# Optimization experiments

Hardware: AMD Instinct MI355X
Metric: run time of the kernel (lower is better)

The kernel has to match this reference:

```python
import jax, jax.numpy as jnp
import numpy as np

S, N, E = 12, 16384, 262144        # timesteps, nodes, edges per timestep
DIN = DOUT = H = 128               # gcn in/out dim == lstm hidden (required by module)
B = 64                             # batch_size; N % B == 0


def setup_inputs() -> dict:
    key = jax.random.key(0)
    ks = jax.random.split(key, 10)
    return {
        "adj_indices": jax.random.randint(ks[0], (S, 2, E), 0, N, dtype=jnp.int32),
        "adj_values": jax.random.uniform(ks[1], (S, E), dtype=jnp.float32),
        "xs": jax.random.normal(ks[2], (S, N, DIN), dtype=jnp.float32),
        "gcn_weight": jax.random.normal(ks[3], (DIN, DOUT), dtype=jnp.float32) * 0.05,
        "gcn_bias": jnp.zeros((DOUT,), jnp.float32),
        "w_ih": jax.random.normal(ks[4], (4 * H, DOUT), dtype=jnp.float32) * 0.05,
        "w_hh": jax.random.normal(ks[5], (4 * H, H), dtype=jnp.float32) * 0.05,
        "b_ih": jnp.zeros((4 * H,), jnp.float32),
        "b_hh": jnp.zeros((4 * H,), jnp.float32),
        "h0": jax.random.normal(ks[6], (B, H), dtype=jnp.float32),
        "c0": jax.random.normal(ks[7], (B, H), dtype=jnp.float32),
    }


def reference(adj_indices, adj_values, xs, gcn_weight, gcn_bias,
              w_ih, w_hh, b_ih, b_hh, h0, c0):
    # --- GCN per timestep: relu(sparse_A @ (X @ W) + b) ---
    def gcn(idx, vals, x):
        support = x @ gcn_weight                      # [N, DOUT]
        msg = vals[:, None] * support[idx[1]]         # gather cols -> [E, DOUT]
        out = jax.ops.segment_sum(msg, idx[0], num_segments=N)  # scatter rows
        return jax.nn.relu(out + gcn_bias)

    cur = jax.vmap(gcn)(adj_indices, adj_values, xs)  # [S, N, DOUT]
    seq = cur.reshape(-1, B, DOUT)                    # [T=S*N/B, B, H]

    # --- single-layer LSTM (torch gate order: i, f, g, o) ---
    def step(carry, x_t):
        h, c = carry
        gates = x_t @ w_ih.T + b_ih + h @ w_hh.T + b_hh   # [B, 4H]
        i, f, g, o = jnp.split(gates, 4, axis=-1)
        c = jax.nn.sigmoid(f) * c + jax.nn.sigmoid(i) * jnp.tanh(g)
        h = jax.nn.sigmoid(o) * jnp.tanh(c)
        return (h, c), h

    _, hs = jax.lax.scan(step, (h0, c0), seq)         # [T, B, H]
    return hs
```

## Files before the change

### kernel.cpp

```cpp
#include <hip/hip_runtime.h>
#include <cstdint>
#include <cstddef>

#define SS 12
#define NN 16384
#define EE 262144
#define TT 3072

typedef _Float16 h2_t __attribute__((ext_vector_type(2)));
typedef short bf16x8 __attribute__((ext_vector_type(8)));
typedef float floatx4 __attribute__((ext_vector_type(4)));
typedef unsigned short ushortx8 __attribute__((ext_vector_type(8)));

__device__ __forceinline__ float fast_sig(float x) {
    float e = __builtin_amdgcn_exp2f(-1.442695041f * x);
    return __builtin_amdgcn_rcpf(1.f + e);
}
__device__ __forceinline__ float fast_tanh(float x) {
    float e = __builtin_amdgcn_exp2f(2.885390082f * x);
    return 1.f - 2.f * __builtin_amdgcn_rcpf(e + 1.f);
}
__device__ __forceinline__ unsigned short f2bf(float f) {
    unsigned int x = __float_as_uint(f);
    unsigned int r = (x + 0x7FFFu + ((x >> 16) & 1u)) >> 16;
    return (unsigned short)r;
}
__device__ __forceinline__ float bf2f(unsigned short u) {
    return __uint_as_float(((unsigned int)u) << 16);
}
__device__ __forceinline__ float dpp_xor1(float x) {
    int i = __builtin_amdgcn_mov_dpp(__float_as_int(x), 0xB1, 0xF, 0xF, true);
    return __int_as_float(i);
}
__device__ __forceinline__ float dpp_xor2(float x) {
    int i = __builtin_amdgcn_mov_dpp(__float_as_int(x), 0x4E, 0xF, 0xF, true);
    return __int_as_float(i);
}

__global__ void k_zero(int* __restrict__ p) {
    p[blockIdx.x * 256 + threadIdx.x] = 0;
}

__global__ void k_count(const int* __restrict__ adj, int* __restrict__ counts) {
    int i = blockIdx.x * 256 + threadIdx.x;
    int t = i / EE, e = i - t * EE;
    int dst = adj[(size_t)t * 2 * EE + e];
    atomicAdd(&counts[t * NN + dst], 1);
}

__global__ void k_scan(const int* __restrict__ counts, int* __restrict__ offs,
                       int* __restrict__ cursor) {
    __shared__ int sums[1024];
    int t = blockIdx.x, tid = threadIdx.x;
    const int per = NN / 1024;
    int base = t * NN + tid * per;
    int local[16];
    int s = 0;
#pragma unroll
    for (int i = 0; i < per; i++) { local[i] = counts[base + i]; s += local[i]; }
    sums[tid] = s;
    __syncthreads();
    for (int off = 1; off < 1024; off <<= 1) {
        int v = (tid >= off) ? sums[tid - off] : 0;
        __syncthreads();
        sums[tid] += v;
        __syncthreads();
    }
    int run = sums[tid] - s;
#pragma unroll
    for (int i = 0; i < per; i++) { offs[base + i] = run; cursor[base + i] = run; run += local[i]; }
}

__global__ void k_scatter(const int* __restrict__ adj, const float* __restrict__ vals,
                          int* __restrict__ cursor, int2* __restrict__ edges) {
    int i = blockIdx.x * 256 + threadIdx.x;
    int t = i / EE, e = i - t * EE;
    int dst = adj[(size_t)t * 2 * EE + e];
    int src = adj[(size_t)t * 2 * EE + EE + e];
    float v = vals[(size_t)t * EE + e];
    int p = atomicAdd(&cursor[t * NN + dst], 1);
    edges[(size_t)t * EE + p] = make_int2(src, __float_as_int(v));
}

__global__ __launch_bounds__(256) void k_support(const float* __restrict__ xs,
                                                 const float* __restrict__ W,
                                                 unsigned short* __restrict__ sup) {
    __shared__ float Ash[64][128];
    __shared__ float Wsh[128][128];
    int tid = threadIdx.x;
    size_t rowbase = (size_t)blockIdx.x * 64;
    const float4* xa = (const float4*)(xs + rowbase * 128);
    float4* As = (float4*)&Ash[0][0];
#pragma unroll
    for (int q = 0; q < 8; q++) As[tid + q * 256] = xa[tid + q * 256];
    const float4* wg = (const float4*)W;
    float4* Ws = (float4*)&Wsh[0][0];
#pragma unroll
    for (int q = 0; q < 16; q++) Ws[tid + q * 256] = wg[tid + q * 256];
    __syncthreads();
    int jg = tid & 31, rg = tid >> 5;
    float acc[8][4];
#pragma unroll
    for (int i = 0; i < 8; i++)
#pragma unroll
        for (int j = 0; j < 4; j++) acc[i][j] = 0.f;
    for (int k4 = 0; k4 < 128; k4 += 4) {
        float4 a[8];
#pragma unroll
        for (int i = 0; i < 8; i++) a[i] = *(const float4*)&Ash[rg * 8 + i][k4];
#pragma unroll
        for (int kk = 0; kk < 4; kk++) {
            float4 wv = *(const float4*)&Wsh[k4 + kk][jg * 4];
#pragma unroll
            for (int i = 0; i < 8; i++) {
                float av = (kk == 0) ? a[i].x : (kk == 1) ? a[i].y : (kk == 2) ? a[i].z : a[i].w;
                acc[i][0] += av * wv.x; acc[i][1] += av * wv.y;
                acc[i][2] += av * wv.z; acc[i][3] += av * wv.w;
            }
        }
    }
#pragma unroll
    for (int i = 0; i < 8; i++) {
        ushort4 o;
        o.x = f2bf(acc[i][0]); o.y = f2bf(acc[i][1]);
        o.z = f2bf(acc[i][2]); o.w = f2bf(acc[i][3]);
        *(ushort4*)&sup[(rowbase + rg * 8 + i) * 128 + jg * 4] = o;
    }
}

__global__ __launch_bounds__(256) void k_gather(const int2* __restrict__ edges,
                         const int* __restrict__ offs,
                         const int* __restrict__ ends,
                         const unsigned short* __restrict__ sup,
                         const float* __restrict__ bias,
                         unsigned short* __restrict__ cur) {
    int bn = blockIdx.x * 4 + (threadIdx.x >> 6);
    bn = __builtin_amdgcn_readfirstlane(bn);
    int t = bn >> 14;
    int l = threadIdx.x & 63;
    int beg = offs[bn];
    int end = ends[bn];
    const unsigned short* supt = sup + (size_t)t * NN * 128;
    const int2* eg = edges + (size_t)t * EE;
    float acc0 = 0.f, acc1 = 0.f;
    int p = beg;
    for (; p + 3 < end; p += 4) {
        int2 e0 = eg[p], e1 = eg[p + 1], e2 = eg[p + 2], e3 = eg[p + 3];
        unsigned int u0 = *(const unsigned int*)&supt[(size_t)e0.x * 128 + 2 * l];
        unsigned int u1 = *(const unsigned int*)&supt[(size_t)e1.x * 128 + 2 * l];
        unsigned int u2 = *(const unsigned int*)&supt[(size_t)e2.x * 128 + 2 * l];
        unsigned int u3 = *(const unsigned int*)&supt[(size_t)e3.x * 128 + 2 * l];
        float w0 = __int_as_float(e0.y), w1 = __int_as_float(e1.y);
        float w2 = __int_as_float(e2.y), w3 = __int_as_float(e3.y);
        acc0 += w0 * bf2f((unsigned short)u0); acc1 += w0 * bf2f((unsigned short)(u0 >> 16));
        acc0 += w1 * bf2f((unsigned short)u1); acc1 += w1 * bf2f((unsigned short)(u1 >> 16));
        acc0 += w2 * bf2f((unsigned short)u2); acc1 += w2 * bf2f((unsigned short)(u2 >> 16));
        acc0 += w3 * bf2f((unsigned short)u3); acc1 += w3 * bf2f((unsigned short)(u3 >> 16));
    }
    for (; p < end; p++) {
        int2 e0 = eg[p];
        unsigned int u0 = *(const unsigned int*)&supt[(size_t)e0.x * 128 + 2 * l];
        float w0 = __int_as_float(e0.y);
        acc0 += w0 * bf2f((unsigned short)u0);
        acc1 += w0 * bf2f((unsigned short)(u0 >> 16));
    }
    float r0 = acc0 + bias[2 * l];
    float r1 = acc1 + bias[2 * l + 1];
    ushort2 o;
    o.x = f2bf(r0 > 0.f ? r0 : 0.f);
    o.y = f2bf(r1 > 0.f ? r1 : 0.f);
    *(ushort2*)&cur[(size_t)bn * 128 + 2 * l] = o;
}

__global__ __launch_bounds__(256) void k_xgates(const unsigned short* __restrict__ cur,
                                                const float* __restrict__ wih,
                                                const float* __restrict__ bih,
                                                const float* __restrict__ bhh,
                                                unsigned short* __restrict__ gx) {
    __shared__ __align__(16) unsigned short At[64][136];
    __shared__ __align__(16) unsigned short Bt[64][136];
    int tid = threadIdx.x;
    size_t rowbase = (size_t)blockIdx.x * 64;
    int gbase = blockIdx.y * 64;
#pragma unroll
    for (int q = 0; q < 4; q++) {
        int idx = tid + q * 256;
        int r = idx >> 4;
        int cc = (idx & 15) * 8;
        *(ushortx8*)&At[r][cc] = *(const ushortx8*)&cur[(rowbase + r) * 128 + cc];
    }
#pragma unroll
    for (int q = 0; q < 8; q++) {
        int idx = tid + q * 256;
        int r = idx >> 5;
        int c4 = (idx & 31) * 4;
        float4 v = *(const float4*)&wih[(size_t)(gbase + r) * 128 + c4];
        ushort4 o;
        o.x = f2bf(v.x); o.y = f2bf(v.y); o.z = f2bf(v.z); o.w = f2bf(v.w);
        *(ushort4*)&Bt[r][c4] = o;
    }
    __syncthreads();
    int wave = tid >> 6, lane = tid & 63;
    int m0 = wave * 16;
    int rin = lane & 15;
    int koff = (lane >> 4) * 8;
    floatx4 acc[4];
#pragma unroll
    for (int n = 0; n < 4; n++) acc[n] = (floatx4){0.f, 0.f, 0.f, 0.f};
#pragma unroll
    for (int kc = 0; kc < 4; kc++) {
        bf16x8 a = *(const bf16x8*)&At[m0 + rin][kc * 32 + koff];
#pragma unroll
        for (int n = 0; n < 4; n++) {
            bf16x8 b = *(const bf16x8*)&Bt[n * 16 + rin][kc * 32 + koff];
            acc[n] = __builtin_amdgcn_mfma_f32_16x16x32_bf16(a, b, acc[n], 0, 0, 0);
        }
    }
    int rq = (lane >> 4) * 4;
#pragma unroll
    for (int n = 0; n < 4; n++) {
        int gcol = gbase + n * 16 + rin;
        float bs = bih[gcol] + bhh[gcol];
        int slot = ((gcol & 127) << 2) | (gcol >> 7);
#pragma unroll
        for (int i = 0; i < 4; i++) {
            size_t row = rowbase + m0 + rq + i;
            gx[row * 512 + slot] = f2bf(acc[n][i] + bs);
        }
    }
}

__global__ __launch_bounds__(256, 1) void k_lstm(const unsigned short* __restrict__ gx,
                                                 const float* __restrict__ whh,
                                                 const float* __restrict__ h0,
                                                 const float* __restrict__ c0,
                                                 float* __restrict__ out) {
    __shared__ __align__(16) _Float16 hsh[2][128];
    int b = blockIdx.x, tid = threadIdx.x;
    int Q = tid >> 2;
    int ll = tid & 3;
    int p = (tid >> 1) & 1;
    int j = 2 * Q + p;

    h2_t wreg[8][16];
#pragma unroll
    for (int g8 = 0; g8 < 8; g8++) {
        int row = (g8 & 3) * 128 + 2 * Q + (g8 >> 2);
        const float4* rp = (const float4*)(whh + (size_t)row * 128 + ll * 32);
#pragma unroll
        for (int q4 = 0; q4 < 8; q4++) {
            float4 v = rp[q4];
            h2_t a; a.x = (_Float16)v.x; a.y = (_Float16)v.y;
            h2_t bq; bq.x = (_Float16)v.z; bq.y = (_Float16)v.w;
            wreg[g8][2 * q4] = a; wreg[g8][2 * q4 + 1] = bq;
        }
    }
    float c = c0[(size_t)b * 128 + j];
    if (tid < 128) hsh[0][tid] = (_Float16)h0[(size_t)b * 128 + tid];
    __syncthreads();

    const unsigned short* gxb = gx + (size_t)b * 512 + 4 * j;
    uint2 rg0 = *(const uint2*)(gxb);
    uint2 rg1 = *(const uint2*)(gxb + 32768);
    uint2 rg2 = *(const uint2*)(gxb + 2 * (size_t)32768);

#define LSTM_STEP(T, RD, WR, QIDX)                                          \
    {                                                                       \
        const h2_t* hp_ = (const h2_t*)&hsh[RD][32 * ll];                   \
        h2_t hs_[16];                                                       \
        _Pragma("unroll")                                                   \
        for (int kk = 0; kk < 16; kk++) hs_[kk] = hp_[kk];                  \
        float part_[8];                                                     \
        _Pragma("unroll")                                                   \
        for (int g8 = 0; g8 < 8; g8++) part_[g8] = 0.f;                     \
        _Pragma("unroll")                                                   \
        for (int kk = 0; kk < 16; kk++) {                                   \
            _Pragma("unroll")                                               \
            for (int g8 = 0; g8 < 8; g8++)                                  \
                part_[g8] = __builtin_amdgcn_fdot2(wreg[g8][kk], hs_[kk],   \
                                                   part_[g8], false);       \
        }                                                                   \
        _Pragma("unroll")                                                   \
        for (int g8 = 0; g8 < 8; g8++) part_[g8] += dpp_xor1(part_[g8]);    \
        _Pragma("unroll")                                                   \
        for (int g8 = 0; g8 < 8; g8++) part_[g8] += dpp_xor2(part_[g8]);    \
        float si_ = p ? part_[4] : part_[0];                                \
        float sf_ = p ? part_[5] : part_[1];                                \
        float sg_ = p ? part_[6] : part_[2];                                \
        float so_ = p ? part_[7] : part_[3];                                \
        uint2 gv_ = rg0;                                                    \
        float ri_ = si_ + bf2f((unsigned short)(gv_.x & 0xffffu));          \
        float rf_ = sf_ + bf2f((unsigned short)(gv_.x >> 16));              \
        float rgg_ = sg_ + bf2f((unsigned short)(gv_.y & 0xffffu));         \
        float ro_ = so_ + bf2f((unsigned short)(gv_.y >> 16));              \
        float ai_ = fast_sig(ri_);                                          \
        float af_ = fast_sig(rf_);                                          \
        float ag_ = fast_tanh(rgg_);                                        \
        float ao_ = fast_sig(ro_);                                          \
        c = af_ * c + ai_ * ag_;                                            \
        float hn_ = ao_ * fast_tanh(c);                                     \
        hh8[QIDX] = hn_;                                                    \
        if ((tid & 1) == 0) hsh[WR][j] = (_Float16)hn_;                     \
        rg0 = rg1; rg1 = rg2;                                               \
        {                                                                   \
            int tp_ = ((T) + 3 < TT) ? (T) + 3 : TT - 1;                    \
            rg2 = *(const uint2*)(gxb + (size_t)tp_ * 32768);               \
        }                                                                   \
        __syncthreads();                                                    \
    }

    for (int t8 = 0; t8 < TT; t8 += 8) {
        float hh8[8];
        LSTM_STEP(t8 + 0, 0, 1, 0);
        LSTM_STEP(t8 + 1, 1, 0, 1);
        LSTM_STEP(t8 + 2, 0, 1, 2);
        LSTM_STEP(t8 + 3, 1, 0, 3);
        LSTM_STEP(t8 + 4, 0, 1, 4);
        LSTM_STEP(t8 + 5, 1, 0, 5);
        LSTM_STEP(t8 + 6, 0, 1, 6);
        LSTM_STEP(t8 + 7, 1, 0, 7);
        if ((tid & 1) == 0) {
#pragma unroll
            for (int q = 0; q < 8; q++)
                out[((size_t)(t8 + q) * 64 + b) * 128 + j] = hh8[q];
        }
    }
#undef LSTM_STEP
}

extern "C" void kernel_launch(void* const* d_in, const int* in_sizes, int n_in,
                              void* d_out, int out_size, void* d_ws, size_t ws_size,
                              hipStream_t stream) {
    const int* adj    = (const int*)d_in[0];
    const float* vals = (const float*)d_in[1];
    const float* xs   = (const float*)d_in[2];
    const float* gw   = (const float*)d_in[3];
    const float* gb   = (const float*)d_in[4];
    const float* wih  = (const float*)d_in[5];
    const float* whh  = (const float*)d_in[6];
    const float* bih  = (const float*)d_in[7];
    const float* bhh  = (const float*)d_in[8];
    const float* h0   = (const float*)d_in[9];
    const float* c0   = (const float*)d_in[10];
    float* out = (float*)d_out;

    char* ws = (char*)d_ws;
    unsigned short* cur = (unsigned short*)(ws);
    unsigned short* gx  = (unsigned short*)(ws + 50331648);
    unsigned short* sup = (unsigned short*)(ws + 50331648);
    int* counts         = (int*)(ws + 100663296);
    int* offs           = (int*)(ws + 101449728);
    int* cursor         = (int*)(ws + 102236160);
    int2* edges         = (int2*)(ws + 103022592);

    k_zero<<<(SS * NN) / 256, 256, 0, stream>>>(counts);
    k_count<<<(SS * EE) / 256, 256, 0, stream>>>(adj, counts);
    k_scan<<<SS, 1024, 0, stream>>>(counts, offs, cursor);
    k_scatter<<<(SS * EE) / 256, 256, 0, stream>>>(adj, vals, cursor, edges);
    k_support<<<(SS * NN) / 64, 256, 0, stream>>>(xs, gw, sup);
    k_gather<<<(SS * NN) / 4, 256, 0, stream>>>(edges, offs, cursor, sup, gb, cur);
    k_xgates<<<dim3((SS * NN) / 64, 8), 256, 0, stream>>>(cur, wih, bih, bhh, gx);
    k_lstm<<<64, 256, 0, stream>>>(gx, whh, h0, c0, out);
}
```

Before: 2.330 ms.

## Split LSTM recurrence across 512 threads with per-lane gate activation and DPP exchange

The recurrent LSTM kernel now launches 512 threads per batch row instead of 256. Each thread holds four W_hh row slices instead of eight, which halves the fdot2 work per thread on the serial critical path. Every lane applies one unified sigmoid/tanh activation to its own gate, and the four gate values are swapped between lanes with DPP moves, so each lane no longer computes four activations. In exchange the kernel needs more waves per block and so more per-step barrier synchronisation, and it issues narrower gate loads.

```diff
diff --git a/kernel.cpp b/kernel.cpp
--- a/kernel.cpp
+++ b/kernel.cpp
@@ -12,10 +12,6 @@
 typedef float floatx4 __attribute__((ext_vector_type(4)));
 typedef unsigned short ushortx8 __attribute__((ext_vector_type(8)));
 
-__device__ __forceinline__ float fast_sig(float x) {
-    float e = __builtin_amdgcn_exp2f(-1.442695041f * x);
-    return __builtin_amdgcn_rcpf(1.f + e);
-}
 __device__ __forceinline__ float fast_tanh(float x) {
     float e = __builtin_amdgcn_exp2f(2.885390082f * x);
     return 1.f - 2.f * __builtin_amdgcn_rcpf(e + 1.f);
@@ -34,6 +30,10 @@
 }
 __device__ __forceinline__ float dpp_xor2(float x) {
     int i = __builtin_amdgcn_mov_dpp(__float_as_int(x), 0x4E, 0xF, 0xF, true);
+    return __int_as_float(i);
+}
+__device__ __forceinline__ float dpp_xor3(float x) {
+    int i = __builtin_amdgcn_mov_dpp(__float_as_int(x), 0x1B, 0xF, 0xF, true);
     return __int_as_float(i);
 }
 
@@ -230,81 +230,77 @@
     }
 }
 
-__global__ __launch_bounds__(256, 1) void k_lstm(const unsigned short* __restrict__ gx,
+__global__ __launch_bounds__(512, 2) void k_lstm(const unsigned short* __restrict__ gx,
                                                  const float* __restrict__ whh,
                                                  const float* __restrict__ h0,
                                                  const float* __restrict__ c0,
                                                  float* __restrict__ out) {
     __shared__ __align__(16) _Float16 hsh[2][128];
     int b = blockIdx.x, tid = threadIdx.x;
-    int Q = tid >> 2;
-    int ll = tid & 3;
-    int p = (tid >> 1) & 1;
-    int j = 2 * Q + p;
-
-    h2_t wreg[8][16];
-#pragma unroll
-    for (int g8 = 0; g8 < 8; g8++) {
-        int row = (g8 & 3) * 128 + 2 * Q + (g8 >> 2);
-        const float4* rp = (const float4*)(whh + (size_t)row * 128 + ll * 32);
+    int j = tid >> 2;
+    int q = tid & 3;
+    float K1 = (q == 2) ? -2.885390082f : -1.442695041f;
+    float Aa = (q == 2) ? 2.f : 1.f;
+    float Bb = (q == 2) ? -1.f : 0.f;
+
+    h2_t w[4][16];
+#pragma unroll
+    for (int g = 0; g < 4; g++) {
+        const float4* rp = (const float4*)(whh + (size_t)(g * 128 + j) * 128 + q * 32);
 #pragma unroll
         for (int q4 = 0; q4 < 8; q4++) {
             float4 v = rp[q4];
             h2_t a; a.x = (_Float16)v.x; a.y = (_Float16)v.y;
             h2_t bq; bq.x = (_Float16)v.z; bq.y = (_Float16)v.w;
-            wreg[g8][2 * q4] = a; wreg[g8][2 * q4 + 1] = bq;
+            w[g][2 * q4] = a; w[g][2 * q4 + 1] = bq;
         }
     }
     float c = c0[(size_t)b * 128 + j];
     if (tid < 128) hsh[0][tid] = (_Float16)h0[(size_t)b * 128 + tid];
     __syncthreads();
 
-    const unsigned short* gxb = gx + (size_t)b * 512 + 4 * j;
-    uint2 rg0 = *(const uint2*)(gxb);
-    uint2 rg1 = *(const uint2*)(gxb + 32768);
-    uint2 rg2 = *(const uint2*)(gxb + 2 * (size_t)32768);
+    const unsigned short* gxb = gx + (size_t)b * 512 + tid;
+    unsigned short rg0 = gxb[0];
+    unsigned short rg1 = gxb[32768];
+    unsigned short rg2 = gxb[2 * (size_t)32768];
 
 #define LSTM_STEP(T, RD, WR, QIDX)                                          \
     {                                                                       \
-        const h2_t* hp_ = (const h2_t*)&hsh[RD][32 * ll];                   \
+        const h2_t* hp_ = (const h2_t*)&hsh[RD][32 * q];                    \
         h2_t hs_[16];                                                       \
         _Pragma("unroll")                                                   \
         for (int kk = 0; kk < 16; kk++) hs_[kk] = hp_[kk];                  \
-        float part_[8];                                                     \
-        _Pragma("unroll")                                                   \
-        for (int g8 = 0; g8 < 8; g8++) part_[g8] = 0.f;                     \
+        float part_[4];                                                     \
+        _Pragma("unroll")                                                   \
+        for (int g = 0; g < 4; g++) part_[g] = 0.f;                         \
         _Pragma("unroll")                                                   \
         for (int kk = 0; kk < 16; kk++) {                                   \
             _Pragma("unroll")                                               \
-            for (int g8 = 0; g8 < 8; g8++)                                  \
-                part_[g8] = __builtin_amdgcn_fdot2(wreg[g8][kk], hs_[kk],   \
-                                                   part_[g8], false);       \
+            for (int g = 0; g < 4; g++)                                     \
+                part_[g] = __builtin_amdgcn_fdot2(w[g][kk], hs_[kk],        \
+                                                  part_[g], false);         \
         }                                                                   \
         _Pragma("unroll")                                                   \
-        for (int g8 = 0; g8 < 8; g8++) part_[g8] += dpp_xor1(part_[g8]);    \
-        _Pragma("unroll")                                                   \
-        for (int g8 = 0; g8 < 8; g8++) part_[g8] += dpp_xor2(part_[g8]);    \
-        float si_ = p ? part_[4] : part_[0];                                \
-        float sf_ = p ? part_[5] : part_[1];                                \
-        float sg_ = p ? part_[6] : part_[2];                                \
-        float so_ = p ? part_[7] : part_[3];                                \
-        uint2 gv_ = rg0;                                                    \
-        float ri_ = si_ + bf2f((unsigned short)(gv_.x & 0xffffu));          \
-        float rf_ = sf_ + bf2f((unsigned short)(gv_.x >> 16));              \
-        float rgg_ = sg_ + bf2f((unsigned short)(gv_.y & 0xffffu));         \
-        float ro_ = so_ + bf2f((unsigned short)(gv_.y >> 16));              \
-        float ai_ = fast_sig(ri_);                                          \
-        float af_ = fast_sig(rf_);                                          \
-        float ag_ = fast_tanh(rgg_);                                        \
-        float ao_ = fast_sig(ro_);                                          \
-        c = af_ * c + ai_ * ag_;                                            \
-        float hn_ = ao_ * fast_tanh(c);                                     \
+        for (int g = 0; g < 4; g++) part_[g] += dpp_xor1(part_[g]);         \
+        _Pragma("unroll")                                                   \
+        for (int g = 0; g < 4; g++) part_[g] += dpp_xor2(part_[g]);         \
+        float s01_ = (q & 1) ? part_[1] : part_[0];                         \
+        float s23_ = (q & 1) ? part_[3] : part_[2];                         \
+        float sown_ = (q & 2) ? s23_ : s01_;                                \
+        float x_ = sown_ + bf2f(rg0);                                       \
+        float e_ = __builtin_amdgcn_exp2f(K1 * x_);                         \
+        float act_ = Aa * __builtin_amdgcn_rcpf(1.f + e_) + Bb;             \
+        float f_ = dpp_xor1(act_);                                          \
+        float tg_ = dpp_xor2(act_);                                         \
+        float o_ = dpp_xor3(act_);                                          \
+        c = f_ * c + act_ * tg_;                   \
+        float hn_ = o_ * fast_tanh(c);                                      \
         hh8[QIDX] = hn_;                                                    \
-        if ((tid & 1) == 0) hsh[WR][j] = (_Float16)hn_;                     \
+        if (q == 0) hsh[WR][j] = (_Float16)hn_;                             \
         rg0 = rg1; rg1 = rg2;                                               \
         {                                                                   \
             int tp_ = ((T) + 3 < TT) ? (T) + 3 : TT - 1;                    \
-            rg2 = *(const uint2*)(gxb + (size_t)tp_ * 32768);               \
+            rg2 = gxb[(size_t)tp_ * 32768];                                 \
         }                                                                   \
         __syncthreads();                                                    \
     }
@@ -319,10 +315,10 @@
         LSTM_STEP(t8 + 5, 1, 0, 5);
         LSTM_STEP(t8 + 6, 0, 1, 6);
         LSTM_STEP(t8 + 7, 1, 0, 7);
-        if ((tid & 1) == 0) {
-#pragma unroll
-            for (int q = 0; q < 8; q++)
-                out[((size_t)(t8 + q) * 64 + b) * 128 + j] = hh8[q];
+        if (q == 0) {
+#pragma unroll
+            for (int qq = 0; qq < 8; qq++)
+                out[((size_t)(t8 + qq) * 64 + b) * 128 + j] = hh8[qq];
         }
     }
 #undef LSTM_STEP
@@ -360,5 +356,5 @@
     k_support<<<(SS * NN) / 64, 256, 0, stream>>>(xs, gw, sup);
     k_gather<<<(SS * NN) / 4, 256, 0, stream>>>(edges, offs, cursor, sup, gb, cur);
     k_xgates<<<dim3((SS * NN) / 64, 8), 256, 0, stream>>>(cur, wih, bih, bhh, gx);
-    k_lstm<<<64, 256, 0, stream>>>(gx, whh, h0, c0, out);
-}
+    k_lstm<<<64, 512, 0, stream>>>(gx, whh, h0, c0, out);
+}
```

Measured after the change: 2.379 ms. +2.1%, slower.

## Compute LSTM recurrent matvec with MFMA using 512-thread blocks

Applied to the files above, without the earlier changes.

Replaces the per-thread fdot2 recurrent dot products and DPP cross-lane reductions in the LSTM kernel with MFMA 16x16x32 f16 instructions. The hidden state is broadcast as the A operand and only one output column of the result is used. Blocks grow to 512 threads (8 waves, 16 hidden units each), and each lane holds W_hh fragments as B operands. This targets the serial per-step latency of the recurrence, at the cost of wasted MFMA rows, and the larger block may make the per-step barrier more expensive.

```diff
diff --git a/kernel.cpp b/kernel.cpp
--- a/kernel.cpp
+++ b/kernel.cpp
@@ -8,6 +8,7 @@
 #define TT 3072
 
 typedef _Float16 h2_t __attribute__((ext_vector_type(2)));
+typedef _Float16 f16x8 __attribute__((ext_vector_type(8)));
 typedef short bf16x8 __attribute__((ext_vector_type(8)));
 typedef float floatx4 __attribute__((ext_vector_type(4)));
 typedef unsigned short ushortx8 __attribute__((ext_vector_type(8)));
@@ -27,14 +28,6 @@
 }
 __device__ __forceinline__ float bf2f(unsigned short u) {
     return __uint_as_float(((unsigned int)u) << 16);
-}
-__device__ __forceinline__ float dpp_xor1(float x) {
-    int i = __builtin_amdgcn_mov_dpp(__float_as_int(x), 0xB1, 0xF, 0xF, true);
-    return __int_as_float(i);
-}
-__device__ __forceinline__ float dpp_xor2(float x) {
-    int i = __builtin_amdgcn_mov_dpp(__float_as_int(x), 0x4E, 0xF, 0xF, true);
-    return __int_as_float(i);
 }
 
 __global__ void k_zero(int* __restrict__ p) {
@@ -230,29 +223,34 @@
     }
 }
 
-__global__ __launch_bounds__(256, 1) void k_lstm(const unsigned short* __restrict__ gx,
+__global__ __launch_bounds__(512, 2) void k_lstm(const unsigned short* __restrict__ gx,
                                                  const float* __restrict__ whh,
                                                  const float* __restrict__ h0,
                                                  const float* __restrict__ c0,
                                                  float* __restrict__ out) {
     __shared__ __align__(16) _Float16 hsh[2][128];
     int b = blockIdx.x, tid = threadIdx.x;
-    int Q = tid >> 2;
-    int ll = tid & 3;
-    int p = (tid >> 1) & 1;
-    int j = 2 * Q + p;
-
-    h2_t wreg[8][16];
-#pragma unroll
-    for (int g8 = 0; g8 < 8; g8++) {
-        int row = (g8 & 3) * 128 + 2 * Q + (g8 >> 2);
-        const float4* rp = (const float4*)(whh + (size_t)row * 128 + ll * 32);
-#pragma unroll
-        for (int q4 = 0; q4 < 8; q4++) {
-            float4 v = rp[q4];
-            h2_t a; a.x = (_Float16)v.x; a.y = (_Float16)v.y;
-            h2_t bq; bq.x = (_Float16)v.z; bq.y = (_Float16)v.w;
-            wreg[g8][2 * q4] = a; wreg[g8][2 * q4 + 1] = bq;
+    int w = tid >> 6;
+    int l = tid & 63;
+    int col = l & 15;
+    int kg = l >> 4;
+    int j = w * 16 + col;
+
+    f16x8 bw[4][4];
+#pragma unroll
+    for (int n = 0; n < 4; n++) {
+        const float* rp = whh + (size_t)(n * 128 + j) * 128;
+#pragma unroll
+        for (int kt = 0; kt < 4; kt++) {
+            int k0 = kt * 32 + kg * 8;
+            float4 v0 = *(const float4*)(rp + k0);
+            float4 v1 = *(const float4*)(rp + k0 + 4);
+            f16x8 f;
+            f[0] = (_Float16)v0.x; f[1] = (_Float16)v0.y;
+            f[2] = (_Float16)v0.z; f[3] = (_Float16)v0.w;
+            f[4] = (_Float16)v1.x; f[5] = (_Float16)v1.y;
+            f[6] = (_Float16)v1.z; f[7] = (_Float16)v1.w;
+            bw[n][kt] = f;
         }
     }
     float c = c0[(size_t)b * 128 + j];
@@ -266,41 +264,42 @@
 
 #define LSTM_STEP(T, RD, WR, QIDX)                                          \
     {                                                                       \
-        const h2_t* hp_ = (const h2_t*)&hsh[RD][32 * ll];                   \
-        h2_t hs_[16];                                                       \
-        _Pragma("unroll")                                                   \
-        for (int kk = 0; kk < 16; kk++) hs_[kk] = hp_[kk];                  \
-        float part_[8];                                                     \
-        _Pragma("unroll")                                                   \
-        for (int g8 = 0; g8 < 8; g8++) part_[g8] = 0.f;                     \
-        _Pragma("unroll")                                                   \
-        for (int kk = 0; kk < 16; kk++) {                                   \
-            _Pragma("unroll")                                               \
-            for (int g8 = 0; g8 < 8; g8++)                                  \
-                part_[g8] = __builtin_amdgcn_fdot2(wreg[g8][kk], hs_[kk],   \
-                                                   part_[g8], false);       \
-        }                                                                   \
-        _Pragma("unroll")                                                   \
-        for (int g8 = 0; g8 < 8; g8++) part_[g8] += dpp_xor1(part_[g8]);    \
-        _Pragma("unroll")                                                   \
-        for (int g8 = 0; g8 < 8; g8++) part_[g8] += dpp_xor2(part_[g8]);    \
-        float si_ = p ? part_[4] : part_[0];                                \
-        float sf_ = p ? part_[5] : part_[1];                                \
-        float sg_ = p ? part_[6] : part_[2];                                \
-        float so_ = p ? part_[7] : part_[3];                                \
-        uint2 gv_ = rg0;                                                    \
-        float ri_ = si_ + bf2f((unsigned short)(gv_.x & 0xffffu));          \
-        float rf_ = sf_ + bf2f((unsigned short)(gv_.x >> 16));              \
-        float rgg_ = sg_ + bf2f((unsigned short)(gv_.y & 0xffffu));         \
-        float ro_ = so_ + bf2f((unsigned short)(gv_.y >> 16));              \
+        f16x8 a0_ = *(const f16x8*)&hsh[RD][kg * 8];                        \
+        f16x8 a1_ = *(const f16x8*)&hsh[RD][32 + kg * 8];                   \
+        f16x8 a2_ = *(const f16x8*)&hsh[RD][64 + kg * 8];                   \
+        f16x8 a3_ = *(const f16x8*)&hsh[RD][96 + kg * 8];                   \
+        floatx4 ac0 = (floatx4){0.f, 0.f, 0.f, 0.f};                        \
+        floatx4 ac1 = (floatx4){0.f, 0.f, 0.f, 0.f};                        \
+        floatx4 ac2 = (floatx4){0.f, 0.f, 0.f, 0.f};                        \
+        floatx4 ac3 = (floatx4){0.f, 0.f, 0.f, 0.f};                        \
+        ac0 = __builtin_amdgcn_mfma_f32_16x16x32_f16(a0_, bw[0][0], ac0, 0, 0, 0); \
+        ac1 = __builtin_amdgcn_mfma_f32_16x16x32_f16(a0_, bw[1][0], ac1, 0, 0, 0); \
+        ac2 = __builtin_amdgcn_mfma_f32_16x16x32_f16(a0_, bw[2][0], ac2, 0, 0, 0); \
+        ac3 = __builtin_amdgcn_mfma_f32_16x16x32_f16(a0_, bw[3][0], ac3, 0, 0, 0); \
+        ac0 = __builtin_amdgcn_mfma_f32_16x16x32_f16(a1_, bw[0][1], ac0, 0, 0, 0); \
+        ac1 = __builtin_amdgcn_mfma_f32_16x16x32_f16(a1_, bw[1][1], ac1, 0, 0, 0); \
+        ac2 = __builtin_amdgcn_mfma_f32_16x16x32_f16(a1_, bw[2][1], ac2, 0, 0, 0); \
+        ac3 = __builtin_amdgcn_mfma_f32_16x16x32_f16(a1_, bw[3][1], ac3, 0, 0, 0); \
+        ac0 = __builtin_amdgcn_mfma_f32_16x16x32_f16(a2_, bw[0][2], ac0, 0, 0, 0); \
+        ac1 = __builtin_amdgcn_mfma_f32_16x16x32_f16(a2_, bw[1][2], ac1, 0, 0, 0); \
+        ac2 = __builtin_amdgcn_mfma_f32_16x16x32_f16(a2_, bw[2][2], ac2, 0, 0, 0); \
+        ac3 = __builtin_amdgcn_mfma_f32_16x16x32_f16(a2_, bw[3][2], ac3, 0, 0, 0); \
+        ac0 = __builtin_amdgcn_mfma_f32_16x16x32_f16(a3_, bw[0][3], ac0, 0, 0, 0); \
+        ac1 = __builtin_amdgcn_mfma_f32_16x16x32_f16(a3_, bw[1][3], ac1, 0, 0, 0); \
+        ac2 = __builtin_amdgcn_mfma_f32_16x16x32_f16(a3_, bw[2][3], ac2, 0, 0, 0); \
+        ac3 = __builtin_amdgcn_mfma_f32_16x16x32_f16(a3_, bw[3][3], ac3, 0, 0, 0); \
+        float ri_ = ac0[0] + bf2f((unsigned short)(rg0.x & 0xffffu));       \
+        float rf_ = ac1[0] + bf2f((unsigned short)(rg0.x >> 16));           \
+        float rg_ = ac2[0] + bf2f((unsigned short)(rg0.y & 0xffffu));       \
+        float ro_ = ac3[0] + bf2f((unsigned short)(rg0.y >> 16));           \
         float ai_ = fast_sig(ri_);                                          \
         float af_ = fast_sig(rf_);                                          \
-        float ag_ = fast_tanh(rgg_);                                        \
+        float ag_ = fast_tanh(rg_);                                         \
         float ao_ = fast_sig(ro_);                                          \
         c = af_ * c + ai_ * ag_;                                            \
         float hn_ = ao_ * fast_tanh(c);                                     \
         hh8[QIDX] = hn_;                                                    \
-        if ((tid & 1) == 0) hsh[WR][j] = (_Float16)hn_;                     \
+        if (kg == 0) hsh[WR][j] = (_Float16)hn_;                            \
         rg0 = rg1; rg1 = rg2;                                               \
         {                                                                   \
             int tp_ = ((T) + 3 < TT) ? (T) + 3 : TT - 1;                    \
@@ -319,10 +318,10 @@
         LSTM_STEP(t8 + 5, 1, 0, 5);
         LSTM_STEP(t8 + 6, 0, 1, 6);
         LSTM_STEP(t8 + 7, 1, 0, 7);
-        if ((tid & 1) == 0) {
-#pragma unroll
-            for (int q = 0; q < 8; q++)
-                out[((size_t)(t8 + q) * 64 + b) * 128 + j] = hh8[q];
+        if (kg == 0) {
+#pragma unroll
+            for (int qq = 0; qq < 8; qq++)
+                out[((size_t)(t8 + qq) * 64 + b) * 128 + j] = hh8[qq];
         }
     }
 #undef LSTM_STEP
@@ -360,5 +359,5 @@
     k_support<<<(SS * NN) / 64, 256, 0, stream>>>(xs, gw, sup);
     k_gather<<<(SS * NN) / 4, 256, 0, stream>>>(edges, offs, cursor, sup, gb, cur);
     k_xgates<<<dim3((SS * NN) / 64, 8), 256, 0, stream>>>(cur, wih, bih, bhh, gx);
-    k_lstm<<<64, 256, 0, stream>>>(gx, whh, h0, c0, out);
-}
+    k_lstm<<<64, 512, 0, stream>>>(gx, whh, h0, c0, out);
+}
```

New measurement: 2.291 ms. Within noise of the previous version (-1.7%).
